# Kernel optimization log

Measured on AMD Instinct MI355X. Metric: run time of the kernel, lower is better.

The kernel has to match this reference:

```python
import jax, jax.numpy as jnp
import numpy as np

B, NAG = 8192, 16          # scenes, agents per scene
CIN, CH = 64, 128          # gnn_in_channels, gnn_out_channels
R2 = 8.0 * 8.0             # comm_range squared
BOX = 20.0                 # positions sampled uniformly in [0, BOX]^2


def _lin(k, fi, fo):
    k1, k2 = jax.random.split(k)
    s = 1.0 / np.sqrt(fi)
    W = jax.random.uniform(k1, (fi, fo), jnp.float32, -s, s)
    b = jax.random.uniform(k2, (fo,), jnp.float32, -s, s)
    return W, b


def setup_inputs() -> dict:
    key = jax.random.key(0)
    ks = jax.random.split(key, 10)
    x = jax.random.normal(ks[0], (B * NAG, CIN), jnp.float32)          # VAE mu per agent
    pos = jax.random.uniform(ks[1], (B, NAG, 2), jnp.float32) * BOX    # sensor xy positions
    W_rel1, b_rel1 = _lin(ks[2], CIN, CH)
    W_root1, _ = _lin(ks[3], CIN, CH)
    W_rel2, b_rel2 = _lin(ks[4], CH, CH)
    W_root2, _ = _lin(ks[5], CH, CH)
    Wh1, bh1 = _lin(ks[6], 2 * CH, 64)
    Wh2, bh2 = _lin(ks[7], 64, 32)
    Wh3, bh3 = _lin(ks[8], 32, 16)
    return dict(x=x, pos=pos, W_rel1=W_rel1, b_rel1=b_rel1, W_root1=W_root1,
                W_rel2=W_rel2, b_rel2=b_rel2, W_root2=W_root2,
                Wh1=Wh1, bh1=bh1, Wh2=Wh2, bh2=bh2, Wh3=Wh3, bh3=bh3)


def _graph_conv(h, adj, W_rel, b_rel, W_root):
    # PyG GraphConv (aggr='add'): out_i = W_rel @ sum_{j in N(i)} h_j + b_rel + W_root @ h_i
    nb = adj.shape[0]
    hb = h.reshape(nb, NAG, h.shape[-1])                 # [B, n, C]
    agg = jnp.einsum('bij,bjc->bic', adj, hb)            # neighbor sum within each scene
    return agg.reshape(h.shape[0], -1) @ W_rel + b_rel + h @ W_root


def reference(x, pos, W_rel1, b_rel1, W_root1, W_rel2, b_rel2, W_root2,
              Wh1, bh1, Wh2, bh2, Wh3, bh3):
    # radius_graph (batch-isolated, loop=False) as a per-scene dense mask
    diff = pos[:, :, None, :] - pos[:, None, :, :]       # [B, n, n, 2]
    d2 = jnp.sum(diff * diff, axis=-1)                   # [B, n, n]
    eye = jnp.eye(NAG, dtype=bool)
    adj = ((d2 <= R2) & ~eye).astype(x.dtype)            # [B, n, n]
    # Dropout(p=0.2) omitted (eval / deterministic reference).
    x1 = jax.nn.relu(_graph_conv(x, adj, W_rel1, b_rel1, W_root1))   # named 'x1' (inplace ReLU)
    x2 = jax.nn.relu(_graph_conv(x1, adj, W_rel2, b_rel2, W_root2))  # named 'x2' (inplace ReLU)
    h = jnp.concatenate([x1, x2], axis=-1)               # JumpingKnowledge('cat')
    h = jax.nn.relu(h @ Wh1 + bh1)
    h = jax.nn.relu(h @ Wh2 + bh2)
    out = h @ Wh3 + bh3                                  # [N, 16]
    return out.reshape(B, NAG, 16)
```

## Files before the change

### kernel.cpp

```cpp
#include <hip/hip_runtime.h>

#define NAG 16
#define SPB 4
#define NBLK 2048
#define R2f 64.0f

typedef unsigned short u16;
typedef __attribute__((ext_vector_type(8))) short short8;
typedef __attribute__((ext_vector_type(4))) float f32x4;

#define MFMA(a, b, c) __builtin_amdgcn_mfma_f32_16x16x32_bf16(a, b, c, 0, 0, 0)

#define OFF_B1 0
#define OFF_B2 16384
#define OFF_H1 49152
#define OFF_H2 65536
#define OFF_H3 67584
#define SWZ_UNITS 8512

__device__ __forceinline__ u16 f2b(float f) {
    unsigned u = __float_as_uint(f);
    unsigned r = u + 0x7FFFu + ((u >> 16) & 1u);
    return (u16)(r >> 16);
}
__device__ __forceinline__ unsigned rb(float f) {
    return (__float_as_uint(f) + 0x8000u) >> 16;
}
__device__ __forceinline__ unsigned pk2(float a, float b) {
    return ((__float_as_uint(a) + 0x8000u) >> 16) |
           ((__float_as_uint(b) + 0x8000u) & 0xFFFF0000u);
}

__global__ __launch_bounds__(256) void swizzle_w(
    const float* __restrict__ Wrel1, const float* __restrict__ Wroot1,
    const float* __restrict__ Wrel2, const float* __restrict__ Wroot2,
    const float* __restrict__ Wh1,  const float* __restrict__ Wh2,
    const float* __restrict__ Wh3,  u16* __restrict__ ws)
{
    const int u = blockIdx.x * 256 + threadIdx.x;
    if (u >= SWZ_UNITS) return;
    int v, T, N, ksplit;
    bool perm = false;
    const float *W, *W2;
    u16* dst;
    if (u < 2048)      { v = u;        T = 8; N = 128; ksplit = 64;  W = Wroot1; W2 = Wrel1; dst = ws + OFF_B1 + v * 8; }
    else if (u < 6144) { v = u - 2048; T = 8; N = 128; ksplit = 128; W = Wroot2; W2 = Wrel2; dst = ws + OFF_B2 + v * 8; perm = true; }
    else if (u < 8192) { v = u - 6144; T = 4; N = 64;  ksplit = 1 << 30; W = Wh1; W2 = Wh1; dst = ws + OFF_H1 + v * 8; perm = true; }
    else if (u < 8448) { v = u - 8192; T = 2; N = 32;  ksplit = 1 << 30; W = Wh2; W2 = Wh2; dst = ws + OFF_H2 + v * 8; }
    else               { v = u - 8448; T = 1; N = 16;  ksplit = 1 << 30; W = Wh3; W2 = Wh3; dst = ws + OFF_H3 + v * 8; }
    const int lane = v & 63;
    const int t = (v >> 6) % T;
    const int s = (v >> 6) / T;
    const int n = t * 16 + (lane & 15);
    const int k0 = s * 32 + (lane >> 4) * 8;
    #pragma unroll
    for (int j = 0; j < 8; ++j) {
        const int k = k0 + j;
        const int kl = perm ? ((k & ~31) + ((k & 31) >> 1) + ((k & 1) << 4)) : k;
        const float val = (kl < ksplit) ? W[kl * N + n] : W2[(kl - ksplit) * N + n];
        dst[j] = f2b(val);
    }
}

__device__ __forceinline__ short8 ldfrag(const u16* __restrict__ ws, int off,
                                         int T, int s, int tile, int lane) {
    return *(const short8*)(ws + off + (size_t)(((s * T + tile) * 64 + lane) * 8));
}

__device__ __forceinline__ short8 make_adjA(unsigned m, int q, int odd) {
    union { short8 v; unsigned u[4]; } r;
    const bool on = (q >> 1) == odd;
    const int base = (q & 1) * 8;
    #pragma unroll
    for (int jj = 0; jj < 4; ++jj) {
        const int k0 = base + 2 * jj;
        const unsigned lo = (on && ((m >> k0) & 1u)) ? 0x3F80u : 0u;
        const unsigned hi = (on && ((m >> (k0 + 1)) & 1u)) ? 0x3F80u : 0u;
        r.u[jj] = lo | (hi << 16);
    }
    return r.v;
}

__global__ __launch_bounds__(256) void gnn_fused5(
    const float* __restrict__ x, const float* __restrict__ pos,
    const float* __restrict__ brel1, const float* __restrict__ brel2,
    const float* __restrict__ bh1,  const float* __restrict__ bh2,
    const float* __restrict__ bh3,
    const u16* __restrict__ ws, float* __restrict__ out)
{
    __shared__ __align__(16) u16 pool[26624];
    __shared__ unsigned mask[64];
    u16* const xb  = pool;
    u16* const yT  = pool + 8704;
    u16* const x1b = pool + 17920;

    const int t = threadIdx.x;
    const int wv = t >> 6, lane = t & 63, ln = lane & 15, q = lane >> 4;
    const int c0 = 32 * wv;
    const int n0 = 2 * wv, n1 = 2 * wv + 1;
    const size_t sA = (size_t)blockIdx.x * SPB;

    {
        const int r = t >> 2, co = (t & 3) * 16;
        const float* src = x + (sA * 16 + r) * 64 + co;
        const float4 v0 = *(const float4*)(src);
        const float4 v1 = *(const float4*)(src + 4);
        const float4 v2 = *(const float4*)(src + 8);
        const float4 v3 = *(const float4*)(src + 12);
        uint4 ua, ub;
        ua.x = pk2(v0.x, v0.y); ua.y = pk2(v0.z, v0.w);
        ua.z = pk2(v1.x, v1.y); ua.w = pk2(v1.z, v1.w);
        ub.x = pk2(v2.x, v2.y); ub.y = pk2(v2.z, v2.w);
        ub.z = pk2(v3.x, v3.y); ub.w = pk2(v3.z, v3.w);
        *(uint4*)&xb[r * 136 + co]     = ua;
        *(uint4*)&xb[r * 136 + co + 8] = ub;
    }
    if (t < 64) {
        const int g = t >> 4, a = t & 15;
        const float* pp = pos + (sA + g) * (NAG * 2);
        const float ax = pp[2 * a], ay = pp[2 * a + 1];
        unsigned m = 0;
        for (int j = 0; j < NAG; ++j) {
            const float dx = ax - pp[2 * j], dy = ay - pp[2 * j + 1];
            if (dx * dx + dy * dy <= R2f && j != a) m |= (1u << j);
        }
        mask[g * 16 + a] = m;
    }
    __syncthreads();

    short8 adjA[4];
    #pragma unroll
    for (int g = 0; g < 4; ++g) adjA[g] = make_adjA(mask[g * 16 + ln], q, g & 1);

    {
        short8 Brl[2][2], Bro[2][2], Af[4][2];
        #pragma unroll
        for (int s = 0; s < 2; ++s) {
            Brl[s][0] = ldfrag(ws, OFF_B1, 8, s + 2, n0, lane);
            Brl[s][1] = ldfrag(ws, OFF_B1, 8, s + 2, n1, lane);
        }
        #pragma unroll
        for (int m = 0; m < 4; ++m) {
            Af[m][0] = *(const short8*)&xb[(m * 16 + ln) * 136 + q * 8];
            Af[m][1] = *(const short8*)&xb[(m * 16 + ln) * 136 + 32 + q * 8];
            f32x4 a0 = {0.f, 0.f, 0.f, 0.f}, a1 = a0;
            a0 = MFMA(Af[m][0], Brl[0][0], a0); a0 = MFMA(Af[m][1], Brl[1][0], a0);
            a1 = MFMA(Af[m][0], Brl[0][1], a1); a1 = MFMA(Af[m][1], Brl[1][1], a1);
            uint2 u0; u0.x = pk2(a0[0], a0[1]); u0.y = pk2(a0[2], a0[3]);
            uint2 u1; u1.x = pk2(a1[0], a1[1]); u1.y = pk2(a1[2], a1[3]);
            *(uint2*)&yT[(c0 + ln) * 72 + m * 16 + q * 4]      = u0;
            *(uint2*)&yT[(c0 + 16 + ln) * 72 + m * 16 + q * 4] = u1;
        }
        short8 By[2][2];
        #pragma unroll
        for (int w = 0; w < 2; ++w) {
            By[w][0] = *(const short8*)&yT[(c0 + ln) * 72 + w * 32 + q * 8];
            By[w][1] = *(const short8*)&yT[(c0 + 16 + ln) * 72 + w * 32 + q * 8];
        }
        #pragma unroll
        for (int s = 0; s < 2; ++s) {
            Bro[s][0] = ldfrag(ws, OFF_B1, 8, s, n0, lane);
            Bro[s][1] = ldfrag(ws, OFF_B1, 8, s, n1, lane);
        }
        const float b0 = brel1[c0 + ln], b1 = brel1[c0 + 16 + ln];
        #pragma unroll
        for (int g = 0; g < 4; ++g) {
            f32x4 a0 = {b0, b0, b0, b0}, a1 = {b1, b1, b1, b1};
            a0 = MFMA(Af[g][0], Bro[0][0], a0); a0 = MFMA(Af[g][1], Bro[1][0], a0);
            a1 = MFMA(Af[g][0], Bro[0][1], a1); a1 = MFMA(Af[g][1], Bro[1][1], a1);
            a0 = MFMA(adjA[g], By[g >> 1][0], a0);
            a1 = MFMA(adjA[g], By[g >> 1][1], a1);
            #pragma unroll
            for (int r = 0; r < 4; ++r) {
                const int row = g * 16 + q * 4 + r;
                *(unsigned*)&x1b[row * 136 + c0 + 2 * ln] =
                    pk2(fmaxf(a0[r], 0.f), fmaxf(a1[r], 0.f));
            }
        }
    }
    __syncthreads();

    {
        short8 Brl[4][2];
        #pragma unroll
        for (int s = 0; s < 4; ++s) {
            Brl[s][0] = ldfrag(ws, OFF_B2, 8, s + 4, n0, lane);
            Brl[s][1] = ldfrag(ws, OFF_B2, 8, s + 4, n1, lane);
        }
        #pragma unroll
        for (int m = 0; m < 4; ++m) {
            f32x4 a0 = {0.f, 0.f, 0.f, 0.f}, a1 = a0;
            #pragma unroll
            for (int s = 0; s < 4; ++s) {
                const short8 A = *(const short8*)&x1b[(m * 16 + ln) * 136 + s * 32 + q * 8];
                a0 = MFMA(A, Brl[s][0], a0);
                a1 = MFMA(A, Brl[s][1], a1);
            }
            uint2 u0; u0.x = pk2(a0[0], a0[1]); u0.y = pk2(a0[2], a0[3]);
            uint2 u1; u1.x = pk2(a1[0], a1[1]); u1.y = pk2(a1[2], a1[3]);
            *(uint2*)&yT[(c0 + ln) * 72 + m * 16 + q * 4]      = u0;
            *(uint2*)&yT[(c0 + 16 + ln) * 72 + m * 16 + q * 4] = u1;
        }
        short8 By[2][2];
        #pragma unroll
        for (int w = 0; w < 2; ++w) {
            By[w][0] = *(const short8*)&yT[(c0 + ln) * 72 + w * 32 + q * 8];
            By[w][1] = *(const short8*)&yT[(c0 + 16 + ln) * 72 + w * 32 + q * 8];
        }
        short8 Bro[4][2];
        #pragma unroll
        for (int s = 0; s < 4; ++s) {
            Bro[s][0] = ldfrag(ws, OFF_B2, 8, s, n0, lane);
            Bro[s][1] = ldfrag(ws, OFF_B2, 8, s, n1, lane);
        }
        const float b0 = brel2[c0 + ln], b1 = brel2[c0 + 16 + ln];
        #pragma unroll
        for (int g = 0; g < 4; ++g) {
            f32x4 a0 = {b0, b0, b0, b0}, a1 = {b1, b1, b1, b1};
            #pragma unroll
            for (int s = 0; s < 4; ++s) {
                const short8 A = *(const short8*)&x1b[(g * 16 + ln) * 136 + s * 32 + q * 8];
                a0 = MFMA(A, Bro[s][0], a0);
                a1 = MFMA(A, Bro[s][1], a1);
            }
            a0 = MFMA(adjA[g], By[g >> 1][0], a0);
            a1 = MFMA(adjA[g], By[g >> 1][1], a1);
            #pragma unroll
            for (int r = 0; r < 4; ++r) {
                const int row = g * 16 + q * 4 + r;
                *(unsigned*)&xb[row * 136 + c0 + 2 * ln] =
                    pk2(fmaxf(a0[r], 0.f), fmaxf(a1[r], 0.f));
            }
        }
    }
    __syncthreads();

    {
        short8 Bf[8];
        #pragma unroll
        for (int s = 0; s < 8; ++s) Bf[s] = ldfrag(ws, OFF_H1, 4, s, wv, lane);
        const float b = bh1[wv * 16 + ln];
        #pragma unroll
        for (int m = 0; m < 4; ++m) {
            f32x4 a = {b, b, b, b}, c = {0.f, 0.f, 0.f, 0.f};
            #pragma unroll
            for (int s = 0; s < 4; ++s) {
                const short8 A1 = *(const short8*)&x1b[(m * 16 + ln) * 136 + s * 32 + q * 8];
                const short8 A2 = *(const short8*)&xb[(m * 16 + ln) * 136 + s * 32 + q * 8];
                a = MFMA(A1, Bf[s], a);
                c = MFMA(A2, Bf[s + 4], c);
            }
            #pragma unroll
            for (int r = 0; r < 4; ++r)
                yT[(m * 16 + q * 4 + r) * 72 + wv * 16 + ln] = (u16)rb(fmaxf(a[r] + c[r], 0.f));
        }
    }
    __syncthreads();

    {
        const u16* h1b = yT;
        u16* h2b = x1b;
        const short8 A0 = *(const short8*)&h1b[(wv * 16 + ln) * 72 + q * 8];
        const short8 A1 = *(const short8*)&h1b[(wv * 16 + ln) * 72 + 32 + q * 8];
        #pragma unroll
        for (int nt = 0; nt < 2; ++nt) {
            const short8 B0 = ldfrag(ws, OFF_H2, 2, 0, nt, lane);
            const short8 B1 = ldfrag(ws, OFF_H2, 2, 1, nt, lane);
            const float b = bh2[nt * 16 + ln];
            f32x4 a = {b, b, b, b};
            a = MFMA(A0, B0, a);
            a = MFMA(A1, B1, a);
            #pragma unroll
            for (int r = 0; r < 4; ++r)
                h2b[(wv * 16 + q * 4 + r) * 40 + nt * 16 + ln] = (u16)rb(fmaxf(a[r], 0.f));
        }
        const short8 A = *(const short8*)&h2b[(wv * 16 + ln) * 40 + q * 8];
        const short8 B = ldfrag(ws, OFF_H3, 1, 0, 0, lane);
        const float b = bh3[ln];
        f32x4 a = {b, b, b, b};
        a = MFMA(A, B, a);
        #pragma unroll
        for (int r = 0; r < 4; ++r)
            out[(sA * 16 + wv * 16 + q * 4 + r) * 16 + ln] = a[r];
    }
}

extern "C" void kernel_launch(void* const* d_in, const int* in_sizes, int n_in,
                              void* d_out, int out_size, void* d_ws, size_t ws_size,
                              hipStream_t stream) {
    const float* x      = (const float*)d_in[0];
    const float* pos    = (const float*)d_in[1];
    const float* Wrel1  = (const float*)d_in[2];
    const float* brel1  = (const float*)d_in[3];
    const float* Wroot1 = (const float*)d_in[4];
    const float* Wrel2  = (const float*)d_in[5];
    const float* brel2  = (const float*)d_in[6];
    const float* Wroot2 = (const float*)d_in[7];
    const float* Wh1    = (const float*)d_in[8];
    const float* bh1    = (const float*)d_in[9];
    const float* Wh2    = (const float*)d_in[10];
    const float* bh2    = (const float*)d_in[11];
    const float* Wh3    = (const float*)d_in[12];
    const float* bh3    = (const float*)d_in[13];
    u16* ws = (u16*)d_ws;

    swizzle_w<<<(SWZ_UNITS + 255) / 256, 256, 0, stream>>>(
        Wrel1, Wroot1, Wrel2, Wroot2, Wh1, Wh2, Wh3, ws);
    gnn_fused5<<<NBLK, 256, 0, stream>>>(
        x, pos, brel1, brel2, bh1, bh2, bh3, ws, (float*)d_out);
}
```

Before: 123.8 us.

## Prefetch next-stage weight fragments early and parallelize adjacency mask computation

Moves global loads of weight fragments and biases for each layer to the stage before they are needed, so their latency overlaps the previous stage's MFMA work and barriers. The per-scene radius mask is now computed by all four waves, with pos loaded as float4 vectors into registers, instead of a serial 16-iteration loop in the first wave. The x loads are issued before the mask math. In exchange, more fragments stay live across stages, which raises register pressure and may lower occupancy.

```diff
diff --git a/kernel.cpp b/kernel.cpp
--- a/kernel.cpp
+++ b/kernel.cpp
@@ -100,13 +100,42 @@
     const int n0 = 2 * wv, n1 = 2 * wv + 1;
     const size_t sA = (size_t)blockIdx.x * SPB;
 
-    {
-        const int r = t >> 2, co = (t & 3) * 16;
-        const float* src = x + (sA * 16 + r) * 64 + co;
-        const float4 v0 = *(const float4*)(src);
-        const float4 v1 = *(const float4*)(src + 4);
-        const float4 v2 = *(const float4*)(src + 8);
-        const float4 v3 = *(const float4*)(src + 12);
+    const float* pp = pos + (sA + wv) * (NAG * 2);
+    const float2 own = *(const float2*)(pp + 2 * ln);
+    float4 pv[8];
+    #pragma unroll
+    for (int i = 0; i < 8; ++i) pv[i] = *(const float4*)(pp + 4 * i);
+
+    const int r = t >> 2, co = (t & 3) * 16;
+    const float* src = x + (sA * 16 + r) * 64 + co;
+    const float4 v0 = *(const float4*)(src);
+    const float4 v1 = *(const float4*)(src + 4);
+    const float4 v2 = *(const float4*)(src + 8);
+    const float4 v3 = *(const float4*)(src + 12);
+
+    short8 Brl1[2][2], Bro1[2][2];
+    #pragma unroll
+    for (int s = 0; s < 2; ++s) {
+        Brl1[s][0] = ldfrag(ws, OFF_B1, 8, s + 2, n0, lane);
+        Brl1[s][1] = ldfrag(ws, OFF_B1, 8, s + 2, n1, lane);
+        Bro1[s][0] = ldfrag(ws, OFF_B1, 8, s, n0, lane);
+        Bro1[s][1] = ldfrag(ws, OFF_B1, 8, s, n1, lane);
+    }
+    const float b10 = brel1[c0 + ln], b11 = brel1[c0 + 16 + ln];
+
+    {
+        unsigned m = 0;
+        #pragma unroll
+        for (int i = 0; i < 8; ++i) {
+            const float dx0 = own.x - pv[i].x, dy0 = own.y - pv[i].y;
+            const float dx1 = own.x - pv[i].z, dy1 = own.y - pv[i].w;
+            if (dx0 * dx0 + dy0 * dy0 <= R2f && ln != 2 * i)     m |= 1u << (2 * i);
+            if (dx1 * dx1 + dy1 * dy1 <= R2f && ln != 2 * i + 1) m |= 1u << (2 * i + 1);
+        }
+        if (q == 0) mask[wv * 16 + ln] = m;
+    }
+
+    {
         uint4 ua, ub;
         ua.x = pk2(v0.x, v0.y); ua.y = pk2(v0.z, v0.w);
         ua.z = pk2(v1.x, v1.y); ua.w = pk2(v1.z, v1.w);
@@ -115,37 +144,23 @@
         *(uint4*)&xb[r * 136 + co]     = ua;
         *(uint4*)&xb[r * 136 + co + 8] = ub;
     }
-    if (t < 64) {
-        const int g = t >> 4, a = t & 15;
-        const float* pp = pos + (sA + g) * (NAG * 2);
-        const float ax = pp[2 * a], ay = pp[2 * a + 1];
-        unsigned m = 0;
-        for (int j = 0; j < NAG; ++j) {
-            const float dx = ax - pp[2 * j], dy = ay - pp[2 * j + 1];
-            if (dx * dx + dy * dy <= R2f && j != a) m |= (1u << j);
-        }
-        mask[g * 16 + a] = m;
-    }
     __syncthreads();
 
     short8 adjA[4];
     #pragma unroll
     for (int g = 0; g < 4; ++g) adjA[g] = make_adjA(mask[g * 16 + ln], q, g & 1);
 
-    {
-        short8 Brl[2][2], Bro[2][2], Af[4][2];
-        #pragma unroll
-        for (int s = 0; s < 2; ++s) {
-            Brl[s][0] = ldfrag(ws, OFF_B1, 8, s + 2, n0, lane);
-            Brl[s][1] = ldfrag(ws, OFF_B1, 8, s + 2, n1, lane);
-        }
+    short8 Brl2[4][2];
+
+    {
+        short8 Af[4][2];
         #pragma unroll
         for (int m = 0; m < 4; ++m) {
             Af[m][0] = *(const short8*)&xb[(m * 16 + ln) * 136 + q * 8];
             Af[m][1] = *(const short8*)&xb[(m * 16 + ln) * 136 + 32 + q * 8];
             f32x4 a0 = {0.f, 0.f, 0.f, 0.f}, a1 = a0;
-            a0 = MFMA(Af[m][0], Brl[0][0], a0); a0 = MFMA(Af[m][1], Brl[1][0], a0);
-            a1 = MFMA(Af[m][0], Brl[0][1], a1); a1 = MFMA(Af[m][1], Brl[1][1], a1);
+            a0 = MFMA(Af[m][0], Brl1[0][0], a0); a0 = MFMA(Af[m][1], Brl1[1][0], a0);
+            a1 = MFMA(Af[m][0], Brl1[0][1], a1); a1 = MFMA(Af[m][1], Brl1[1][1], a1);
             uint2 u0; u0.x = pk2(a0[0], a0[1]); u0.y = pk2(a0[2], a0[3]);
             uint2 u1; u1.x = pk2(a1[0], a1[1]); u1.y = pk2(a1[2], a1[3]);
             *(uint2*)&yT[(c0 + ln) * 72 + m * 16 + q * 4]      = u0;
@@ -158,34 +173,36 @@
             By[w][1] = *(const short8*)&yT[(c0 + 16 + ln) * 72 + w * 32 + q * 8];
         }
         #pragma unroll
-        for (int s = 0; s < 2; ++s) {
-            Bro[s][0] = ldfrag(ws, OFF_B1, 8, s, n0, lane);
-            Bro[s][1] = ldfrag(ws, OFF_B1, 8, s, n1, lane);
-        }
-        const float b0 = brel1[c0 + ln], b1 = brel1[c0 + 16 + ln];
+        for (int s = 0; s < 4; ++s) {
+            Brl2[s][0] = ldfrag(ws, OFF_B2, 8, s + 4, n0, lane);
+            Brl2[s][1] = ldfrag(ws, OFF_B2, 8, s + 4, n1, lane);
+        }
         #pragma unroll
         for (int g = 0; g < 4; ++g) {
-            f32x4 a0 = {b0, b0, b0, b0}, a1 = {b1, b1, b1, b1};
-            a0 = MFMA(Af[g][0], Bro[0][0], a0); a0 = MFMA(Af[g][1], Bro[1][0], a0);
-            a1 = MFMA(Af[g][0], Bro[0][1], a1); a1 = MFMA(Af[g][1], Bro[1][1], a1);
+            f32x4 a0 = {b10, b10, b10, b10}, a1 = {b11, b11, b11, b11};
+            a0 = MFMA(Af[g][0], Bro1[0][0], a0); a0 = MFMA(Af[g][1], Bro1[1][0], a0);
+            a1 = MFMA(Af[g][0], Bro1[0][1], a1); a1 = MFMA(Af[g][1], Bro1[1][1], a1);
             a0 = MFMA(adjA[g], By[g >> 1][0], a0);
             a1 = MFMA(adjA[g], By[g >> 1][1], a1);
             #pragma unroll
-            for (int r = 0; r < 4; ++r) {
-                const int row = g * 16 + q * 4 + r;
+            for (int r2 = 0; r2 < 4; ++r2) {
+                const int row = g * 16 + q * 4 + r2;
                 *(unsigned*)&x1b[row * 136 + c0 + 2 * ln] =
-                    pk2(fmaxf(a0[r], 0.f), fmaxf(a1[r], 0.f));
+                    pk2(fmaxf(a0[r2], 0.f), fmaxf(a1[r2], 0.f));
             }
         }
     }
     __syncthreads();
 
-    {
-        short8 Brl[4][2];
+    short8 Bf[8];
+
+    {
+        const float b20 = brel2[c0 + ln], b21 = brel2[c0 + 16 + ln];
+        short8 Bro2[4][2];
         #pragma unroll
         for (int s = 0; s < 4; ++s) {
-            Brl[s][0] = ldfrag(ws, OFF_B2, 8, s + 4, n0, lane);
-            Brl[s][1] = ldfrag(ws, OFF_B2, 8, s + 4, n1, lane);
+            Bro2[s][0] = ldfrag(ws, OFF_B2, 8, s, n0, lane);
+            Bro2[s][1] = ldfrag(ws, OFF_B2, 8, s, n1, lane);
         }
         #pragma unroll
         for (int m = 0; m < 4; ++m) {
@@ -193,8 +210,8 @@
             #pragma unroll
             for (int s = 0; s < 4; ++s) {
                 const short8 A = *(const short8*)&x1b[(m * 16 + ln) * 136 + s * 32 + q * 8];
-                a0 = MFMA(A, Brl[s][0], a0);
-                a1 = MFMA(A, Brl[s][1], a1);
+                a0 = MFMA(A, Brl2[s][0], a0);
+                a1 = MFMA(A, Brl2[s][1], a1);
             }
             uint2 u0; u0.x = pk2(a0[0], a0[1]); u0.y = pk2(a0[2], a0[3]);
             uint2 u1; u1.x = pk2(a1[0], a1[1]); u1.y = pk2(a1[2], a1[3]);
@@ -207,38 +224,41 @@
             By[w][0] = *(const short8*)&yT[(c0 + ln) * 72 + w * 32 + q * 8];
             By[w][1] = *(const short8*)&yT[(c0 + 16 + ln) * 72 + w * 32 + q * 8];
         }
-        short8 Bro[4][2];
-        #pragma unroll
-        for (int s = 0; s < 4; ++s) {
-            Bro[s][0] = ldfrag(ws, OFF_B2, 8, s, n0, lane);
-            Bro[s][1] = ldfrag(ws, OFF_B2, 8, s, n1, lane);
-        }
-        const float b0 = brel2[c0 + ln], b1 = brel2[c0 + 16 + ln];
+        #pragma unroll
+        for (int s = 0; s < 8; ++s)
+            Bf[s] = ldfrag(ws, OFF_H1, 4, s, wv, lane);
         #pragma unroll
         for (int g = 0; g < 4; ++g) {
-            f32x4 a0 = {b0, b0, b0, b0}, a1 = {b1, b1, b1, b1};
+            f32x4 a0 = {b20, b20, b20, b20}, a1 = {b21, b21, b21, b21};
             #pragma unroll
             for (int s = 0; s < 4; ++s) {
                 const short8 A = *(const short8*)&x1b[(g * 16 + ln) * 136 + s * 32 + q * 8];
-                a0 = MFMA(A, Bro[s][0], a0);
-                a1 = MFMA(A, Bro[s][1], a1);
+                a0 = MFMA(A, Bro2[s][0], a0);
+                a1 = MFMA(A, Bro2[s][1], a1);
             }
             a0 = MFMA(adjA[g], By[g >> 1][0], a0);
             a1 = MFMA(adjA[g], By[g >> 1][1], a1);
             #pragma unroll
-            for (int r = 0; r < 4; ++r) {
-                const int row = g * 16 + q * 4 + r;
+            for (int r2 = 0; r2 < 4; ++r2) {
+                const int row = g * 16 + q * 4 + r2;
                 *(unsigned*)&xb[row * 136 + c0 + 2 * ln] =
-                    pk2(fmaxf(a0[r], 0.f), fmaxf(a1[r], 0.f));
+                    pk2(fmaxf(a0[r2], 0.f), fmaxf(a1[r2], 0.f));
             }
         }
     }
     __syncthreads();
 
-    {
-        short8 Bf[8];
-        #pragma unroll
-        for (int s = 0; s < 8; ++s) Bf[s] = ldfrag(ws, OFF_H1, 4, s, wv, lane);
+    short8 Bg2[2][2], Bg3;
+    float hb2[2], hb3;
+    {
+        #pragma unroll
+        for (int nt = 0; nt < 2; ++nt) {
+            Bg2[0][nt] = ldfrag(ws, OFF_H2, 2, 0, nt, lane);
+            Bg2[1][nt] = ldfrag(ws, OFF_H2, 2, 1, nt, lane);
+        }
+        Bg3 = ldfrag(ws, OFF_H3, 1, 0, 0, lane);
+        hb2[0] = bh2[ln]; hb2[1] = bh2[16 + ln]; hb3 = bh3[ln];
+
         const float b = bh1[wv * 16 + ln];
         #pragma unroll
         for (int m = 0; m < 4; ++m) {
@@ -251,8 +271,8 @@
                 c = MFMA(A2, Bf[s + 4], c);
             }
             #pragma unroll
-            for (int r = 0; r < 4; ++r)
-                yT[(m * 16 + q * 4 + r) * 72 + wv * 16 + ln] = (u16)rb(fmaxf(a[r] + c[r], 0.f));
+            for (int r2 = 0; r2 < 4; ++r2)
+                yT[(m * 16 + q * 4 + r2) * 72 + wv * 16 + ln] = (u16)rb(fmaxf(a[r2] + c[r2], 0.f));
         }
     }
     __syncthreads();
@@ -264,24 +284,20 @@
         const short8 A1 = *(const short8*)&h1b[(wv * 16 + ln) * 72 + 32 + q * 8];
         #pragma unroll
         for (int nt = 0; nt < 2; ++nt) {
-            const short8 B0 = ldfrag(ws, OFF_H2, 2, 0, nt, lane);
-            const short8 B1 = ldfrag(ws, OFF_H2, 2, 1, nt, lane);
-            const float b = bh2[nt * 16 + ln];
+            const float b = hb2[nt];
             f32x4 a = {b, b, b, b};
-            a = MFMA(A0, B0, a);
-            a = MFMA(A1, B1, a);
-            #pragma unroll
-            for (int r = 0; r < 4; ++r)
-                h2b[(wv * 16 + q * 4 + r) * 40 + nt * 16 + ln] = (u16)rb(fmaxf(a[r], 0.f));
+            a = MFMA(A0, Bg2[0][nt], a);
+            a = MFMA(A1, Bg2[1][nt], a);
+            #pragma unroll
+            for (int r2 = 0; r2 < 4; ++r2)
+                h2b[(wv * 16 + q * 4 + r2) * 40 + nt * 16 + ln] = (u16)rb(fmaxf(a[r2], 0.f));
         }
         const short8 A = *(const short8*)&h2b[(wv * 16 + ln) * 40 + q * 8];
-        const short8 B = ldfrag(ws, OFF_H3, 1, 0, 0, lane);
-        const float b = bh3[ln];
-        f32x4 a = {b, b, b, b};
-        a = MFMA(A, B, a);
-        #pragma unroll
-        for (int r = 0; r < 4; ++r)
-            out[(sA * 16 + wv * 16 + q * 4 + r) * 16 + ln] = a[r];
+        f32x4 a = {hb3, hb3, hb3, hb3};
+        a = MFMA(A, Bg3, a);
+        #pragma unroll
+        for (int r2 = 0; r2 < 4; ++r2)
+            out[(sA * 16 + wv * 16 + q * 4 + r2) * 16 + ln] = a[r2];
     }
 }
 
```

New measurement: 125.3 us. No clear change (+1.2%).
